# Kernel tuning notes

Hardware: AMD Instinct MI355X
Metric: run time of the kernel (lower is better)

Reference implementation:

```python
import jax, jax.numpy as jnp
import numpy as np

G, N, E, B = 4, 100000, 500000, 512
V, D, H, C = 50000, 300, 128, 20
NUM_HEADS, STEPS = 3, 2


def setup_inputs() -> dict:
    key = jax.random.key(0)
    ks = jax.random.split(key, 12)
    return {
        "node_indices": jax.random.randint(ks[0], (G, N), 0, V),
        "src": jax.random.randint(ks[1], (G, E), 0, N),
        "dst": jax.random.randint(ks[2], (G, E), 0, N),
        "node_graph_ids": jnp.sort(jax.random.randint(ks[3], (G, N), 0, B), axis=-1),
        "edge_weights": jax.random.uniform(ks[4], (G, E), dtype=jnp.float32),
        "emb_table": jax.random.normal(ks[5], (V, D), dtype=jnp.float32) * 0.1,
        "edge_params": jnp.ones((G,), dtype=jnp.float32),
        "W_proj": jax.random.normal(ks[6], (G, D, H), dtype=jnp.float32) / np.sqrt(D),
        "b_proj": jnp.zeros((G, H), dtype=jnp.float32),
        "W_cls": jax.random.normal(ks[7], (G, H, C), dtype=jnp.float32) / np.sqrt(H),
        "b_cls": jnp.zeros((G, C), dtype=jnp.float32),
        "W_fuse": jax.random.normal(ks[8], (NUM_HEADS, C, C, G), dtype=jnp.float32) / np.sqrt(C * G),
        "b_fuse": jnp.zeros((NUM_HEADS, C), dtype=jnp.float32),
    }


def _per_graph_logits(idx, s, d, gid, ew, emb_table, ep, Wp, bp, Wc, bc):
    # embedding lookup + input projection: [N, H]
    h = emb_table[idx] @ Wp + bp
    # graph_learning: relu(scalar * edge_weights)
    w = jax.nn.relu(ep * ew)  # [E]
    # in-degree for DGL mean reduce (0 in-edges -> 0 agg)
    deg = jax.ops.segment_sum(jnp.ones_like(ew), d, num_segments=N)
    inv_deg = jnp.where(deg > 0, 1.0 / deg, 0.0)[:, None]  # [N, 1]
    for _ in range(STEPS):
        msg = h[s] * w[:, None]                                   # gather-multiply [E, H]
        agg = jax.ops.segment_sum(msg, d, num_segments=N) * inv_deg  # scatter-mean [N, H]
        h = h + agg
    # dgl.mean_nodes: per-document mean of node features
    cnt = jax.ops.segment_sum(jnp.ones((N,), h.dtype), gid, num_segments=B)
    doc = jax.ops.segment_sum(h, gid, num_segments=B) / jnp.maximum(cnt, 1.0)[:, None]  # [B, H]
    # classify (dropout = identity in eval)
    return jax.nn.relu(doc) @ Wc + bc  # [B, C]


def reference(node_indices, src, dst, node_graph_ids, edge_weights, emb_table,
              edge_params, W_proj, b_proj, W_cls, b_cls, W_fuse, b_fuse):
    per_graph = jax.vmap(_per_graph_logits,
                         in_axes=(0, 0, 0, 0, 0, None, 0, 0, 0, 0, 0))
    logits = per_graph(node_indices, src, dst, node_graph_ids, edge_weights,
                       emb_table, edge_params, W_proj, b_proj, W_cls, b_cls)  # [G, B, C]
    stacked = jnp.transpose(logits, (1, 2, 0))  # [B, C_in, G] (Conv1d input, kernel=G)
    # Conv1d(out=C, in=C, k=G) per head, valid -> length 1, squeezed
    head_out = jnp.einsum('big,hoig->hbo', stacked, W_fuse) + b_fuse[:, None, :]  # [NH, B, C]
    fused_logits = head_out.mean(axis=0)  # [B, C]
    predictions = jax.nn.softmax(fused_logits, axis=-1)
    return predictions, fused_logits
```

## Files before the change

kernel.cpp:

```cpp
#include <hip/hip_runtime.h>

#define G_  4
#define N_  100000
#define E_  500000
#define B_  512
#define V_  50000
#define D_  300
#define H_  128
#define C_  20
#define NH_ 3

#define KP_  320
#define SCB_  512
#define NBLK_ ((N_ + SCB_ - 1) / SCB_)

typedef unsigned short ushort_t;
typedef __attribute__((ext_vector_type(8))) short bf16x8;
typedef __attribute__((ext_vector_type(4))) float f32x4;

__device__ __forceinline__ ushort_t f2bf(float f) {
    unsigned int x = __float_as_uint(f);
    unsigned int r = x + 0x7FFFu + ((x >> 16) & 1u);
    return (ushort_t)(r >> 16);
}

__device__ __forceinline__ int lower_bound_i(const int* __restrict__ a, int n, int v) {
    int lo = 0, hi = n;
    while (lo < hi) {
        int mid = (lo + hi) >> 1;
        if (a[mid] < v) lo = mid + 1; else hi = mid;
    }
    return lo;
}

__device__ __forceinline__ void unpack8(uint4 u, float* f) {
    f[0] = __uint_as_float((u.x & 0xFFFFu) << 16);
    f[1] = __uint_as_float(u.x & 0xFFFF0000u);
    f[2] = __uint_as_float((u.y & 0xFFFFu) << 16);
    f[3] = __uint_as_float(u.y & 0xFFFF0000u);
    f[4] = __uint_as_float((u.z & 0xFFFFu) << 16);
    f[5] = __uint_as_float(u.z & 0xFFFF0000u);
    f[6] = __uint_as_float((u.w & 0xFFFFu) << 16);
    f[7] = __uint_as_float(u.w & 0xFFFF0000u);
}

__global__ __launch_bounds__(256) void convert_w_kernel(
    const float* __restrict__ Wp,
    ushort_t* __restrict__ Wt)
{
    int flat = blockIdx.x * 256 + threadIdx.x;
    int g = flat / (H_ * KP_);
    int r = flat % (H_ * KP_);
    int n = r / KP_;
    int k = r % KP_;
    float v = (k < D_) ? Wp[((size_t)g * D_ + k) * H_ + n] : 0.f;
    Wt[flat] = f2bf(v);
}

__global__ __launch_bounds__(256) void mfma_gemm_kernel(
    const float* __restrict__ emb,
    const ushort_t* __restrict__ Wt,
    const float* __restrict__ bp,
    ushort_t* __restrict__ Ph)
{
    const int g    = blockIdx.x;
    const int row0 = blockIdx.y * 128;
    const int w    = threadIdx.x >> 6;
    const int l    = threadIdx.x & 63;
    const int l16  = l & 15;
    const int lk   = (l >> 4) * 8;

    const ushort_t* Wg = Wt + (size_t)g * H_ * KP_;
    ushort_t*       Pg = Ph + (size_t)g * V_ * H_;

    f32x4 acc[2][8];
#pragma unroll
    for (int m = 0; m < 2; ++m)
#pragma unroll
        for (int n = 0; n < 8; ++n) acc[m][n] = (f32x4){0.f, 0.f, 0.f, 0.f};

    const int wrow = row0 + w * 32;
    int arow[2];
    arow[0] = min(wrow + l16,      V_ - 1);
    arow[1] = min(wrow + 16 + l16, V_ - 1);

    for (int kp0 = 0; kp0 < KP_; kp0 += 32) {
        const int kb = kp0 + lk;

        bf16x8 a[2];
#pragma unroll
        for (int m = 0; m < 2; ++m) {
            float v[8];
            const float* ap = &emb[(size_t)arow[m] * D_ + kb];
            if (kb + 8 <= D_) {
                float4 x0 = *reinterpret_cast<const float4*>(ap);
                float4 x1 = *reinterpret_cast<const float4*>(ap + 4);
                v[0] = x0.x; v[1] = x0.y; v[2] = x0.z; v[3] = x0.w;
                v[4] = x1.x; v[5] = x1.y; v[6] = x1.z; v[7] = x1.w;
            } else {
#pragma unroll
                for (int j = 0; j < 8; ++j)
                    v[j] = (kb + j < D_) ? ap[j] : 0.f;
            }
#pragma unroll
            for (int j = 0; j < 8; ++j) a[m][j] = (short)f2bf(v[j]);
        }

        bf16x8 b[8];
#pragma unroll
        for (int n = 0; n < 8; ++n)
            b[n] = *reinterpret_cast<const bf16x8*>(&Wg[(size_t)(n * 16 + l16) * KP_ + kb]);

#pragma unroll
        for (int m = 0; m < 2; ++m)
#pragma unroll
            for (int n = 0; n < 8; ++n)
                acc[m][n] = __builtin_amdgcn_mfma_f32_16x16x32_bf16(
                    a[m], b[n], acc[m][n], 0, 0, 0);
    }

    const int rbase = (l >> 4) * 4;
#pragma unroll
    for (int n = 0; n < 8; ++n) {
        const int col  = n * 16 + l16;
        const float bv = bp[g * H_ + col];
#pragma unroll
        for (int m = 0; m < 2; ++m) {
#pragma unroll
            for (int r = 0; r < 4; ++r) {
                int row = wrow + m * 16 + rbase + r;
                if (row < V_)
                    Pg[(size_t)row * H_ + col] = f2bf(acc[m][n][r] + bv);
            }
        }
    }
}

__global__ __launch_bounds__(256) void deg_count_kernel(const int* __restrict__ dstA,
                                                        int* __restrict__ deg)
{
    const int g = blockIdx.y;
    int e = blockIdx.x * 256 + threadIdx.x;
    if (e < E_) atomicAdd(&deg[g * N_ + dstA[(size_t)g * E_ + e]], 1);
}

__global__ __launch_bounds__(512) void scan1_kernel(const int* __restrict__ deg,
                                                    int* __restrict__ bsum)
{
    __shared__ int sh[512];
    const int g = blockIdx.y, b = blockIdx.x, t = threadIdx.x;
    int i = b * SCB_ + t;
    sh[t] = (i < N_) ? deg[g * N_ + i] : 0;
    __syncthreads();
#pragma unroll
    for (int ofs = 256; ofs > 0; ofs >>= 1) {
        if (t < ofs) sh[t] += sh[t + ofs];
        __syncthreads();
    }
    if (t == 0) bsum[g * NBLK_ + b] = sh[0];
}

__global__ __launch_bounds__(256) void scan2_kernel(const int* __restrict__ bsum,
                                                    int* __restrict__ bpre,
                                                    int* __restrict__ off)
{
    __shared__ int sh[256];
    const int g = blockIdx.x, t = threadIdx.x;
    int v = (t < NBLK_) ? bsum[g * NBLK_ + t] : 0;
    sh[t] = v;
    __syncthreads();
#pragma unroll
    for (int ofs = 1; ofs < 256; ofs <<= 1) {
        int u = (t >= ofs) ? sh[t - ofs] : 0;
        __syncthreads();
        sh[t] += u;
        __syncthreads();
    }
    if (t < NBLK_) bpre[g * (NBLK_ + 1) + t + 1] = sh[t];
    if (t == 0) {
        bpre[g * (NBLK_ + 1)] = 0;
        off[(size_t)g * (N_ + 1) + N_] = sh[NBLK_ - 1];
    }
}

__global__ __launch_bounds__(512) void scan3_kernel(int* __restrict__ deg,
                                                    const int* __restrict__ bpre,
                                                    int* __restrict__ off)
{
    __shared__ int sh[512];
    const int g = blockIdx.y, b = blockIdx.x, t = threadIdx.x;
    int i = b * SCB_ + t;
    int v = (i < N_) ? deg[g * N_ + i] : 0;
    sh[t] = v;
    __syncthreads();
#pragma unroll
    for (int ofs = 1; ofs < 512; ofs <<= 1) {
        int u = (t >= ofs) ? sh[t - ofs] : 0;
        __syncthreads();
        sh[t] += u;
        __syncthreads();
    }
    if (i < N_) {
        off[(size_t)g * (N_ + 1) + i] = bpre[g * (NBLK_ + 1) + b] + sh[t] - v;
        deg[g * N_ + i] = 0;
    }
}

__global__ __launch_bounds__(256) void scatter_kernel(
    const int* __restrict__ srcA, const int* __restrict__ dstA,
    const float* __restrict__ ewA, const float* __restrict__ ep,
    const int* __restrict__ idxA, const int* __restrict__ off,
    int* __restrict__ cnt, int4* __restrict__ csr4)
{
    const int g = blockIdx.y;
    int e = blockIdx.x * 256 + threadIdx.x;
    if (e >= E_) return;
    int s = srcA[(size_t)g * E_ + e];
    int d = dstA[(size_t)g * E_ + e];
    int pos = off[(size_t)g * (N_ + 1) + d] + atomicAdd(&cnt[g * N_ + d], 1);
    float w = ep[g] * ewA[(size_t)g * E_ + e];
    csr4[(size_t)g * E_ + pos] =
        make_int4(s, idxA[(size_t)g * N_ + s], __float_as_int(fmaxf(w, 0.f)), 0);
}

__global__ __launch_bounds__(256) void prop1_kernel(
    const int* __restrict__ idx_g, const int* __restrict__ off,
    const int4* __restrict__ csr4,
    const ushort_t* __restrict__ Ph, ushort_t* __restrict__ hBh)
{
    const int n = blockIdx.x * 16 + (threadIdx.x >> 4);
    if (n >= N_) return;
    const int lane = threadIdx.x & 15;
    const int col  = lane * 8;

    const int lo = off[n], hi = off[n + 1];

    float sf[8];
    unpack8(*reinterpret_cast<const uint4*>(&Ph[(size_t)idx_g[n] * H_ + col]), sf);

    float acc[8];
#pragma unroll
    for (int j = 0; j < 8; ++j) acc[j] = 0.f;

    int i = lo;
    for (; i + 4 <= hi; i += 4) {
        int4 e0 = csr4[i],     e1 = csr4[i + 1];
        int4 e2 = csr4[i + 2], e3 = csr4[i + 3];
        float c0 = __int_as_float(e0.z), c1 = __int_as_float(e1.z);
        float c2 = __int_as_float(e2.z), c3 = __int_as_float(e3.z);
        uint4 u0 = *reinterpret_cast<const uint4*>(&Ph[(size_t)e0.y * H_ + col]);
        uint4 u1 = *reinterpret_cast<const uint4*>(&Ph[(size_t)e1.y * H_ + col]);
        uint4 u2 = *reinterpret_cast<const uint4*>(&Ph[(size_t)e2.y * H_ + col]);
        uint4 u3 = *reinterpret_cast<const uint4*>(&Ph[(size_t)e3.y * H_ + col]);
        float f0[8], f1[8], f2[8], f3[8];
        unpack8(u0, f0); unpack8(u1, f1); unpack8(u2, f2); unpack8(u3, f3);
#pragma unroll
        for (int j = 0; j < 8; ++j)
            acc[j] += c0 * f0[j] + c1 * f1[j] + c2 * f2[j] + c3 * f3[j];
    }
    for (; i < hi; ++i) {
        int4 e0 = csr4[i];
        float c = __int_as_float(e0.z);
        float f[8];
        unpack8(*reinterpret_cast<const uint4*>(&Ph[(size_t)e0.y * H_ + col]), f);
#pragma unroll
        for (int j = 0; j < 8; ++j) acc[j] += c * f[j];
    }

    const float inv = (hi > lo) ? 1.0f / (float)(hi - lo) : 0.f;
    ushort_t p[8];
#pragma unroll
    for (int j = 0; j < 8; ++j) p[j] = f2bf(sf[j] + inv * acc[j]);
    uint4 o;
    o.x = (unsigned)p[0] | ((unsigned)p[1] << 16);
    o.y = (unsigned)p[2] | ((unsigned)p[3] << 16);
    o.z = (unsigned)p[4] | ((unsigned)p[5] << 16);
    o.w = (unsigned)p[6] | ((unsigned)p[7] << 16);
    *reinterpret_cast<uint4*>(&hBh[(size_t)n * H_ + col]) = o;
}

__global__ __launch_bounds__(256) void prop2_fused_kernel(
    const int* __restrict__ off, const int4* __restrict__ csr4,
    const int* __restrict__ gid,
    const ushort_t* __restrict__ hBh, float* __restrict__ docsum)
{
    const int nloc = threadIdx.x >> 4;
    const int n    = blockIdx.x * 16 + nloc;
    const int lane = threadIdx.x & 15;
    const int col  = lane * 8;

    __shared__ float sh[16][H_];
    __shared__ int   shgid[16];

    float o[8];
    if (n < N_) {
        const int lo = off[n], hi = off[n + 1];

        float sf[8];
        unpack8(*reinterpret_cast<const uint4*>(&hBh[(size_t)n * H_ + col]), sf);

        float acc[8];
#pragma unroll
        for (int j = 0; j < 8; ++j) acc[j] = 0.f;

        int i = lo;
        for (; i + 4 <= hi; i += 4) {
            int4 e0 = csr4[i],     e1 = csr4[i + 1];
            int4 e2 = csr4[i + 2], e3 = csr4[i + 3];
            float c0 = __int_as_float(e0.z), c1 = __int_as_float(e1.z);
            float c2 = __int_as_float(e2.z), c3 = __int_as_float(e3.z);
            uint4 u0 = *reinterpret_cast<const uint4*>(&hBh[(size_t)e0.x * H_ + col]);
            uint4 u1 = *reinterpret_cast<const uint4*>(&hBh[(size_t)e1.x * H_ + col]);
            uint4 u2 = *reinterpret_cast<const uint4*>(&hBh[(size_t)e2.x * H_ + col]);
            uint4 u3 = *reinterpret_cast<const uint4*>(&hBh[(size_t)e3.x * H_ + col]);
            float f0[8], f1[8], f2[8], f3[8];
            unpack8(u0, f0); unpack8(u1, f1); unpack8(u2, f2); unpack8(u3, f3);
#pragma unroll
            for (int j = 0; j < 8; ++j)
                acc[j] += c0 * f0[j] + c1 * f1[j] + c2 * f2[j] + c3 * f3[j];
        }
        for (; i < hi; ++i) {
            int4 e0 = csr4[i];
            float c = __int_as_float(e0.z);
            float f[8];
            unpack8(*reinterpret_cast<const uint4*>(&hBh[(size_t)e0.x * H_ + col]), f);
#pragma unroll
            for (int j = 0; j < 8; ++j) acc[j] += c * f[j];
        }

        const float inv = (hi > lo) ? 1.0f / (float)(hi - lo) : 0.f;
#pragma unroll
        for (int j = 0; j < 8; ++j) o[j] = sf[j] + inv * acc[j];
        if (lane == 0) shgid[nloc] = gid[n];
    } else {
#pragma unroll
        for (int j = 0; j < 8; ++j) o[j] = 0.f;
        if (lane == 0) shgid[nloc] = -1;
    }

#pragma unroll
    for (int j = 0; j < 8; ++j) sh[nloc][col + j] = o[j];
    __syncthreads();

    const int c  = threadIdx.x & 127;
    const int q  = threadIdx.x >> 7;
    const int n0 = q * 8;
    float run = 0.f;
    int rgid = shgid[n0];
    for (int k = 0; k < 8; ++k) {
        int gk = shgid[n0 + k];
        if (gk != rgid) {
            if (rgid >= 0) atomicAdd(&docsum[(size_t)rgid * H_ + c], run);
            run = 0.f; rgid = gk;
        }
        run += sh[n0 + k][c];
    }
    if (rgid >= 0) atomicAdd(&docsum[(size_t)rgid * H_ + c], run);
}

__global__ __launch_bounds__(128) void cls_kernel(
    const int* __restrict__ gidA, const float* __restrict__ docsum,
    const float* __restrict__ Wc, const float* __restrict__ bc,
    float* __restrict__ logits)
{
    const int b   = blockIdx.x;
    const int g   = blockIdx.y;
    const int tid = threadIdx.x;
    const int* gid = gidA + (size_t)g * N_;

    int lo = lower_bound_i(gid, N_, b);
    int hi = lower_bound_i(gid, N_, b + 1);
    float cnt = (float)(hi - lo);

    __shared__ float sdoc[H_];
    float dv = docsum[((size_t)g * B_ + b) * H_ + tid] / fmaxf(cnt, 1.0f);
    sdoc[tid] = fmaxf(dv, 0.f);
    __syncthreads();

    if (tid < C_) {
        const float* Wcg = Wc + (size_t)g * H_ * C_;
        float acc = bc[g * C_ + tid];
#pragma unroll 8
        for (int hh = 0; hh < H_; ++hh) acc += sdoc[hh] * Wcg[hh * C_ + tid];
        logits[((size_t)g * B_ + b) * C_ + tid] = acc;
    }
}

__global__ __launch_bounds__(64) void fuse_kernel(
    const float* __restrict__ logits,
    const float* __restrict__ Wf,
    const float* __restrict__ bf,
    float* __restrict__ out)
{
    const int b   = blockIdx.x;
    const int tid = threadIdx.x;

    __shared__ float s[C_ * G_];
    __shared__ float fl[C_];

    for (int t = tid; t < C_ * G_; t += 64) {
        int i = t >> 2, g = t & 3;
        s[t] = logits[((long)g * B_ + b) * C_ + i];
    }
    __syncthreads();

    if (tid < C_) {
        float acc = 0.f;
        for (int hd = 0; hd < NH_; ++hd) {
            float a = bf[hd * C_ + tid];
            const float* wrow = &Wf[((hd * C_ + tid) * C_) * G_];
#pragma unroll 5
        for (int i = 0; i < C_; ++i) {
#pragma unroll
                for (int g = 0; g < G_; ++g)
                    a += s[i * G_ + g] * wrow[i * G_ + g];
            }
            acc += a;
        }
        fl[tid] = acc * (1.0f / 3.0f);
    }
    __syncthreads();

    if (tid < C_) {
        float f = fl[tid];
        float m = -1e30f;
#pragma unroll
        for (int i = 0; i < C_; ++i) m = fmaxf(m, fl[i]);
        float ssum = 0.f;
#pragma unroll
        for (int i = 0; i < C_; ++i) ssum += expf(fl[i] - m);
        out[b * C_ + tid] = expf(f - m) / ssum;
        out[B_ * C_ + b * C_ + tid] = f;
    }
}

extern "C" void kernel_launch(void* const* d_in, const int* in_sizes, int n_in,
                              void* d_out, int out_size, void* d_ws, size_t ws_size,
                              hipStream_t stream)
{
    const int*   node_indices = (const int*)d_in[0];
    const int*   srcA         = (const int*)d_in[1];
    const int*   dstA         = (const int*)d_in[2];
    const int*   gidA         = (const int*)d_in[3];
    const float* ewA          = (const float*)d_in[4];
    const float* emb          = (const float*)d_in[5];
    const float* ep           = (const float*)d_in[6];
    const float* Wp           = (const float*)d_in[7];
    const float* bp           = (const float*)d_in[8];
    const float* Wc           = (const float*)d_in[9];
    const float* bc           = (const float*)d_in[10];
    const float* Wf           = (const float*)d_in[11];
    const float* bf           = (const float*)d_in[12];
    float*       out          = (float*)d_out;

    char* wp0 = (char*)d_ws;
    auto alloc = [&](size_t bytes) {
        void* r = (void*)wp0;
        wp0 += (bytes + 255) & ~(size_t)255;
        return r;
    };
    ushort_t* hBh      = (ushort_t*)alloc((size_t)N_ * H_ * 2);
    float*    docsum   = (float*)   alloc((size_t)G_ * B_ * H_ * 4);
    float*    logits   = (float*)   alloc((size_t)G_ * B_ * C_ * 4);
    ushort_t* Wt       = (ushort_t*)alloc((size_t)G_ * H_ * KP_ * 2);
    int*      deg_i    = (int*)     alloc((size_t)G_ * N_ * 4);
    int*      off      = (int*)     alloc((size_t)G_ * (N_ + 1) * 4);
    int*      bsum     = (int*)     alloc((size_t)G_ * NBLK_ * 4);
    int*      bpre     = (int*)     alloc((size_t)G_ * (NBLK_ + 1) * 4);
    int4*     csr4     = (int4*)    alloc((size_t)G_ * E_ * 16);

    const size_t pbytes = (size_t)V_ * H_ * 2;
    size_t used  = (size_t)(wp0 - (char*)d_ws);
    size_t avail = (ws_size > used) ? ws_size - used : 0;

    int ng;
    if (avail >= 4 * pbytes + 1024)      ng = 4;
    else if (avail >= 2 * pbytes + 1024) ng = 2;
    else                                 ng = 1;
    ushort_t* Ph = (ushort_t*)alloc((size_t)ng * pbytes);

    convert_w_kernel<<<(G_ * H_ * KP_) / 256, 256, 0, stream>>>(Wp, Wt);
    hipMemsetAsync(docsum, 0, (size_t)G_ * B_ * H_ * sizeof(float), stream);

    hipMemsetAsync(deg_i, 0, (size_t)G_ * N_ * sizeof(int), stream);
    deg_count_kernel<<<dim3((E_ + 255) / 256, G_), 256, 0, stream>>>(dstA, deg_i);
    scan1_kernel<<<dim3(NBLK_, G_), 512, 0, stream>>>(deg_i, bsum);
    scan2_kernel<<<G_, 256, 0, stream>>>(bsum, bpre, off);
    scan3_kernel<<<dim3(NBLK_, G_), 512, 0, stream>>>(deg_i, bpre, off);
    scatter_kernel<<<dim3((E_ + 255) / 256, G_), 256, 0, stream>>>(
        srcA, dstA, ewA, ep, node_indices, off, deg_i, csr4);

    for (int gbase = 0; gbase < G_; gbase += ng) {
        mfma_gemm_kernel<<<dim3(ng, (V_ + 127) / 128), 256, 0, stream>>>(
            emb, Wt + (size_t)gbase * H_ * KP_, bp + (size_t)gbase * H_, Ph);

        for (int gi = 0; gi < ng; ++gi) {
            const int g = gbase + gi;
            const int*      idx   = node_indices + (size_t)g * N_;
            const int*      gid   = gidA + (size_t)g * N_;
            const int*      off_g = off + (size_t)g * (N_ + 1);
            const int4*     csr_g = csr4 + (size_t)g * E_;
            const ushort_t* Pg    = Ph + (size_t)gi * V_ * H_;

            prop1_kernel<<<(N_ + 15) / 16, 256, 0, stream>>>(
                idx, off_g, csr_g, Pg, hBh);
            prop2_fused_kernel<<<(N_ + 15) / 16, 256, 0, stream>>>(
                off_g, csr_g, gid, hBh, docsum + (size_t)g * B_ * H_);
        }
    }

    cls_kernel<<<dim3(B_, G_), 128, 0, stream>>>(gidA, docsum, Wc, bc, logits);
    fuse_kernel<<<B_, 64, 0, stream>>>(logits, Wf, bf, out);
}
```

Measured before the change: 548.8 us.

## Share embedding A-tile across all graphs in one GEMM block and prefetch next K slice

The projection GEMM now computes all NG graphs' weight products in one block, so each embedding row tile is loaded from global memory and converted to bf16 once instead of once per graph. Each block covers 64 rows, with waves split across row halves and column halves. The next K slice of A is loaded in software-pipelined fashion before the current MFMAs run. The accumulator footprint grows with NG (up to 128 floats per lane), which may raise register pressure and lower occupancy.

```diff
diff --git a/kernel.cpp b/kernel.cpp
--- a/kernel.cpp
+++ b/kernel.cpp
@@ -57,37 +57,33 @@
     Wt[flat] = f2bf(v);
 }
 
-__global__ __launch_bounds__(256) void mfma_gemm_kernel(
+template <int NG>
+__global__ __launch_bounds__(256) void mfma_gemm_multi_kernel(
     const float* __restrict__ emb,
     const ushort_t* __restrict__ Wt,
     const float* __restrict__ bp,
     ushort_t* __restrict__ Ph)
 {
-    const int g    = blockIdx.x;
-    const int row0 = blockIdx.y * 128;
     const int w    = threadIdx.x >> 6;
     const int l    = threadIdx.x & 63;
     const int l16  = l & 15;
     const int lk   = (l >> 4) * 8;
-
-    const ushort_t* Wg = Wt + (size_t)g * H_ * KP_;
-    ushort_t*       Pg = Ph + (size_t)g * V_ * H_;
-
-    f32x4 acc[2][8];
-#pragma unroll
-    for (int m = 0; m < 2; ++m)
-#pragma unroll
-        for (int n = 0; n < 8; ++n) acc[m][n] = (f32x4){0.f, 0.f, 0.f, 0.f};
-
-    const int wrow = row0 + w * 32;
+    const int rb   = blockIdx.x * 64 + (w & 1) * 32;
+    const int ch   = (w >> 1) * 64;
+
+    f32x4 acc[NG][2][4];
+#pragma unroll
+    for (int g = 0; g < NG; ++g)
+#pragma unroll
+        for (int m = 0; m < 2; ++m)
+#pragma unroll
+            for (int n = 0; n < 4; ++n) acc[g][m][n] = (f32x4){0.f, 0.f, 0.f, 0.f};
+
     int arow[2];
-    arow[0] = min(wrow + l16,      V_ - 1);
-    arow[1] = min(wrow + 16 + l16, V_ - 1);
-
-    for (int kp0 = 0; kp0 < KP_; kp0 += 32) {
-        const int kb = kp0 + lk;
-
-        bf16x8 a[2];
+    arow[0] = min(rb + l16,      V_ - 1);
+    arow[1] = min(rb + 16 + l16, V_ - 1);
+
+    auto load_a = [&](int kb, bf16x8* a) {
 #pragma unroll
         for (int m = 0; m < 2; ++m) {
             float v[8];
@@ -105,32 +101,50 @@
 #pragma unroll
             for (int j = 0; j < 8; ++j) a[m][j] = (short)f2bf(v[j]);
         }
-
-        bf16x8 b[8];
-#pragma unroll
-        for (int n = 0; n < 8; ++n)
-            b[n] = *reinterpret_cast<const bf16x8*>(&Wg[(size_t)(n * 16 + l16) * KP_ + kb]);
-
-#pragma unroll
-        for (int m = 0; m < 2; ++m)
-#pragma unroll
-            for (int n = 0; n < 8; ++n)
-                acc[m][n] = __builtin_amdgcn_mfma_f32_16x16x32_bf16(
-                    a[m], b[n], acc[m][n], 0, 0, 0);
+    };
+
+    bf16x8 aCur[2], aNxt[2];
+    load_a(lk, aCur);
+
+    for (int kp0 = 0; kp0 < KP_; kp0 += 32) {
+        const int kb = kp0 + lk;
+        if (kp0 + 32 < KP_) load_a(kb + 32, aNxt);
+
+#pragma unroll
+        for (int g = 0; g < NG; ++g) {
+            const ushort_t* Wg = Wt + (size_t)g * H_ * KP_;
+            bf16x8 b[4];
+#pragma unroll
+            for (int n = 0; n < 4; ++n)
+                b[n] = *reinterpret_cast<const bf16x8*>(
+                    &Wg[(size_t)(ch + n * 16 + l16) * KP_ + kb]);
+#pragma unroll
+            for (int m = 0; m < 2; ++m)
+#pragma unroll
+                for (int n = 0; n < 4; ++n)
+                    acc[g][m][n] = __builtin_amdgcn_mfma_f32_16x16x32_bf16(
+                        aCur[m], b[n], acc[g][m][n], 0, 0, 0);
+        }
+        aCur[0] = aNxt[0];
+        aCur[1] = aNxt[1];
     }
 
     const int rbase = (l >> 4) * 4;
 #pragma unroll
-    for (int n = 0; n < 8; ++n) {
-        const int col  = n * 16 + l16;
-        const float bv = bp[g * H_ + col];
-#pragma unroll
-        for (int m = 0; m < 2; ++m) {
-#pragma unroll
-            for (int r = 0; r < 4; ++r) {
-                int row = wrow + m * 16 + rbase + r;
-                if (row < V_)
-                    Pg[(size_t)row * H_ + col] = f2bf(acc[m][n][r] + bv);
+    for (int g = 0; g < NG; ++g) {
+        ushort_t* Pg = Ph + (size_t)g * V_ * H_;
+#pragma unroll
+        for (int n = 0; n < 4; ++n) {
+            const int col  = ch + n * 16 + l16;
+            const float bv = bp[g * H_ + col];
+#pragma unroll
+            for (int m = 0; m < 2; ++m) {
+#pragma unroll
+                for (int r = 0; r < 4; ++r) {
+                    int row = rb + m * 16 + rbase + r;
+                    if (row < V_)
+                        Pg[(size_t)row * H_ + col] = f2bf(acc[g][m][n][r] + bv);
+                }
             }
         }
     }
@@ -490,9 +504,16 @@
     scatter_kernel<<<dim3((E_ + 255) / 256, G_), 256, 0, stream>>>(
         srcA, dstA, ewA, ep, node_indices, off, deg_i, csr4);
 
+    const int gemm_blocks = (V_ + 63) / 64;
     for (int gbase = 0; gbase < G_; gbase += ng) {
-        mfma_gemm_kernel<<<dim3(ng, (V_ + 127) / 128), 256, 0, stream>>>(
-            emb, Wt + (size_t)gbase * H_ * KP_, bp + (size_t)gbase * H_, Ph);
+        const ushort_t* Wtg = Wt + (size_t)gbase * H_ * KP_;
+        const float*    bpg = bp + (size_t)gbase * H_;
+        if (ng == 4)
+            mfma_gemm_multi_kernel<4><<<gemm_blocks, 256, 0, stream>>>(emb, Wtg, bpg, Ph);
+        else if (ng == 2)
+            mfma_gemm_multi_kernel<2><<<gemm_blocks, 256, 0, stream>>>(emb, Wtg, bpg, Ph);
+        else
+            mfma_gemm_multi_kernel<1><<<gemm_blocks, 256, 0, stream>>>(emb, Wtg, bpg, Ph);
 
         for (int gi = 0; gi < ng; ++gi) {
             const int g = gbase + gi;
```

After: 592.3 us. 7.9% more time.
